# Optimization experiments

Hardware: AMD Instinct MI355X
Metric: run time of the kernel (lower is better)

The kernel has to match this reference:

```python
import jax, jax.numpy as jnp
import numpy as np

N = 50000
E = 800000
IN_CH = 128
HID = 16
HEADS = 16
OUT_CH = 64
NEG_SLOPE = 0.2
EPS = 1e-16


def _add_self_loops(edge_index, n):
    loops = jnp.arange(n, dtype=edge_index.dtype)
    src = jnp.concatenate([edge_index[0], loops])
    dst = jnp.concatenate([edge_index[1], loops])
    return src, dst


def gat_conv(x, src, dst, W, a_src, a_dst, b, heads, out_ch, concat, n):
    # x: [N, F_in], W: [F_in, heads*out_ch], a_src/a_dst: [heads, out_ch]
    h = (x @ W).reshape(n, heads, out_ch)                 # [N, H, C]
    alpha_src = jnp.sum(h * a_src, axis=-1)               # [N, H]
    alpha_dst = jnp.sum(h * a_dst, axis=-1)               # [N, H]
    e = alpha_src[src] + alpha_dst[dst]                   # [E, H]
    e = jnp.where(e > 0, e, NEG_SLOPE * e)                # LeakyReLU(0.2)
    m = jax.ops.segment_max(e, dst, num_segments=n)       # [N, H] (finite: self-loops)
    ex = jnp.exp(e - m[dst])                              # [E, H]
    denom = jax.ops.segment_sum(ex, dst, num_segments=n)  # [N, H]
    alpha = ex / (denom[dst] + EPS)                       # [E, H]
    msg = h[src] * alpha[:, :, None]                      # [E, H, C]
    out = jax.ops.segment_sum(msg, dst, num_segments=n)   # [N, H, C]
    if concat:
        out = out.reshape(n, heads * out_ch)
    else:
        out = out.mean(axis=1)
    return out + b


def setup_inputs() -> dict:
    key = jax.random.key(0)
    ks = jax.random.split(key, 10)
    x = jax.random.normal(ks[0], (N, IN_CH), dtype=jnp.float32)
    edge_index = jax.random.randint(ks[1], (2, E), 0, N, dtype=jnp.int64)
    s1 = 1.0 / np.sqrt(IN_CH)
    W1 = jax.random.normal(ks[2], (IN_CH, HEADS * HID), dtype=jnp.float32) * s1
    a_src1 = jax.random.normal(ks[3], (HEADS, HID), dtype=jnp.float32) * (1.0 / np.sqrt(HID))
    a_dst1 = jax.random.normal(ks[4], (HEADS, HID), dtype=jnp.float32) * (1.0 / np.sqrt(HID))
    b1 = jnp.zeros((HEADS * HID,), dtype=jnp.float32)
    s2 = 1.0 / np.sqrt(HEADS * HID)
    W2 = jax.random.normal(ks[5], (HEADS * HID, OUT_CH), dtype=jnp.float32) * s2
    a_src2 = jax.random.normal(ks[6], (1, OUT_CH), dtype=jnp.float32) * (1.0 / np.sqrt(OUT_CH))
    a_dst2 = jax.random.normal(ks[7], (1, OUT_CH), dtype=jnp.float32) * (1.0 / np.sqrt(OUT_CH))
    b2 = jnp.zeros((OUT_CH,), dtype=jnp.float32)
    return {"x": x, "edge_index": edge_index, "W1": W1, "a_src1": a_src1,
            "a_dst1": a_dst1, "b1": b1, "W2": W2, "a_src2": a_src2,
            "a_dst2": a_dst2, "b2": b2}


def reference(x, edge_index, W1, a_src1, a_dst1, b1, W2, a_src2, a_dst2, b2):
    src, dst = _add_self_loops(edge_index, N)
    h = gat_conv(x, src, dst, W1, a_src1, a_dst1, b1, HEADS, HID, True, N)
    h = gat_conv(h, src, dst, W2, a_src2, a_dst2, b2, 1, OUT_CH, False, N)
    return jax.nn.sigmoid(h)
```

## Files before the change

kernel.cpp:

```cpp
#include <hip/hip_runtime.h>
#include <hip/hip_bf16.h>

#define NN 50000
#define EE 800000
#define TE 850000
#define BK 64
#define NGB 782
#define NEB 1661

typedef __hip_bfloat16 bf16;
typedef __attribute__((ext_vector_type(8))) short short8v;
typedef __attribute__((ext_vector_type(4))) float float4v;

__device__ __forceinline__ float bu2f(unsigned short v) {
    return __uint_as_float((unsigned)v << 16);
}
__device__ __forceinline__ unsigned short f2bu(float v) {
    bf16 t = __float2bfloat16(v);
    return *(unsigned short*)&t;
}
__device__ __forceinline__ float lrelu(float e) { return (e > 0.f) ? e : 0.2f * e; }
__device__ __forceinline__ int clampn(int v) {
    return (v < 0) ? 0 : (v >= NN ? NN - 1 : v);
}

__global__ __launch_bounds__(256) void wprep_k(
    const float* __restrict__ W1, const float* __restrict__ W2,
    const float* __restrict__ asr1, const float* __restrict__ ads1,
    const float* __restrict__ asr2, const float* __restrict__ ads2,
    unsigned short* __restrict__ W1T, unsigned short* __restrict__ W2T,
    unsigned short* __restrict__ P1sT, unsigned short* __restrict__ P1dT,
    unsigned short* __restrict__ P2T, int* __restrict__ deg) {
    int b = blockIdx.x, t = threadIdx.x;
    for (int i = b * 256 + t; i < NN; i += 256 * 256) deg[i] = 0;
    if (b < 128) {
        int j = b * 256 + t;
        int n = j >> 7, k = j & 127;
        W1T[j] = f2bu(W1[k * 256 + n]);
    } else if (b < 192) {
        int j = (b - 128) * 256 + t;
        int n = j >> 8, k = j & 255;
        W2T[j] = f2bu(W2[k * 64 + n]);
    } else if (b == 192) {
        for (int j = t; j < 2048; j += 256) {
            int h = j >> 7, k = j & 127;
            float s = 0.f, d = 0.f;
            for (int c = 0; c < 16; ++c) {
                float wv = W1[k * 256 + h * 16 + c];
                s += wv * asr1[h * 16 + c];
                d += wv * ads1[h * 16 + c];
            }
            P1sT[j] = f2bu(s);
            P1dT[j] = f2bu(d);
        }
    } else if (b == 193) {
        int k = t;
        float s = 0.f, d = 0.f;
        for (int c = 0; c < 64; ++c) {
            float wv = W2[k * 64 + c];
            s += wv * asr2[c];
            d += wv * ads2[c];
        }
        P2T[k] = f2bu(s);
        P2T[256 + k] = f2bu(d);
        for (int j = 512 + t; j < 4096; j += 256) P2T[j] = 0;
    }
}

__global__ __launch_bounds__(256) void eg1_k(
    const void* __restrict__ ei, const float* __restrict__ x,
    const unsigned short* __restrict__ W1T,
    const unsigned short* __restrict__ P1sT, const unsigned short* __restrict__ P1dT,
    int* __restrict__ deg, int* __restrict__ csr,
    bf16* __restrict__ h1, float* __restrict__ a_src, float* __restrict__ a_dst) {
    if (blockIdx.x < NGB) {
        int wv = threadIdx.x >> 6, lane = threadIdx.x & 63;
        int m = lane & 15, quad = lane >> 4;
        int row0 = blockIdx.x * 64 + wv * 16;
        int arow = row0 + m;
        int arowc = (arow < NN) ? arow : NN - 1;
        const float4* x4 = (const float4*)x;
        short8v a[4];
#pragma unroll
        for (int ks = 0; ks < 4; ++ks) {
            float4 f0 = x4[(size_t)arowc * 32 + ks * 8 + quad * 2];
            float4 f1 = x4[(size_t)arowc * 32 + ks * 8 + quad * 2 + 1];
            union { short8v v; unsigned short u[8]; } ua;
            ua.u[0] = f2bu(f0.x); ua.u[1] = f2bu(f0.y);
            ua.u[2] = f2bu(f0.z); ua.u[3] = f2bu(f0.w);
            ua.u[4] = f2bu(f1.x); ua.u[5] = f2bu(f1.y);
            ua.u[6] = f2bu(f1.z); ua.u[7] = f2bu(f1.w);
            a[ks] = ua.v;
        }
        float4v accs = {0.f, 0.f, 0.f, 0.f}, accd = {0.f, 0.f, 0.f, 0.f};
#pragma unroll
        for (int ks = 0; ks < 4; ++ks) {
            short8v bs = *(const short8v*)&P1sT[(size_t)m * 128 + quad * 8 + ks * 32];
            short8v bd = *(const short8v*)&P1dT[(size_t)m * 128 + quad * 8 + ks * 32];
            accs = __builtin_amdgcn_mfma_f32_16x16x32_bf16(a[ks], bs, accs, 0, 0, 0);
            accd = __builtin_amdgcn_mfma_f32_16x16x32_bf16(a[ks], bd, accd, 0, 0, 0);
        }
        float4v acc[16];
#pragma unroll
        for (int t = 0; t < 16; ++t) {
            float4v c = {0.f, 0.f, 0.f, 0.f};
            const unsigned short* wb = &W1T[(size_t)(t * 16 + m) * 128 + quad * 8];
#pragma unroll
            for (int ks = 0; ks < 4; ++ks) {
                short8v b = *(const short8v*)&wb[ks * 32];
                c = __builtin_amdgcn_mfma_f32_16x16x32_bf16(a[ks], b, c, 0, 0, 0);
            }
            acc[t] = c;
        }
#pragma unroll
        for (int t = 0; t < 16; ++t) {
#pragma unroll
            for (int r = 0; r < 4; ++r) {
                int orow = row0 + quad * 4 + r;
                if (orow < NN)
                    h1[(size_t)orow * 256 + t * 16 + m] = __float2bfloat16(acc[t][r]);
            }
        }
#pragma unroll
        for (int r = 0; r < 4; ++r) {
            int orow = row0 + quad * 4 + r;
            if (orow < NN) {
                a_src[orow * 16 + m] = accs[r];
                a_dst[orow * 16 + m] = accd[r];
            }
        }
        return;
    }
    __shared__ int sflag;
    int t = threadIdx.x;
    if (t < 64) {
        unsigned z = (((const unsigned*)ei)[2 * t + 1] == 0u) ? 1u : 0u;
        unsigned long long mb = __ballot(z);
        if (t == 0) sflag = (__popcll(mb) >= 32) ? 1 : 0;
    }
    __syncthreads();
    int isi64 = sflag;
    int p = (blockIdx.x - NGB) * 256 + t;
    int i0 = p * 2;
    if (i0 >= TE) return;
    int s0, d0, s1 = -1, d1 = -1;
    if (i0 + 1 < EE) {
        if (isi64) {
            longlong2 sv = ((const longlong2*)ei)[p];
            longlong2 dv = ((const longlong2*)ei)[(EE >> 1) + p];
            s0 = clampn((int)sv.x); s1 = clampn((int)sv.y);
            d0 = clampn((int)dv.x); d1 = clampn((int)dv.y);
        } else {
            int2 sv = ((const int2*)ei)[p];
            int2 dv = ((const int2*)ei)[(EE >> 1) + p];
            s0 = clampn(sv.x); s1 = clampn(sv.y);
            d0 = clampn(dv.x); d1 = clampn(dv.y);
        }
    } else {
        auto lde = [&](long long idx) {
            return clampn(isi64 ? (int)((const long long*)ei)[idx] : ((const int*)ei)[idx]);
        };
        if (i0 < EE) { s0 = lde(i0); d0 = lde((long long)EE + i0); }
        else         { s0 = i0 - EE; d0 = i0 - EE; }
        if (i0 + 1 < TE) {
            if (i0 + 1 < EE) { s1 = lde(i0 + 1); d1 = lde((long long)EE + i0 + 1); }
            else             { s1 = i0 + 1 - EE; d1 = i0 + 1 - EE; }
        }
    }
    int pos0 = atomicAdd(&deg[d0], 1);
    if (pos0 < BK) csr[d0 * BK + pos0] = s0;
    if (d1 >= 0) {
        int pos1 = atomicAdd(&deg[d1], 1);
        if (pos1 < BK) csr[d1 * BK + pos1] = s1;
    }
}

__global__ __launch_bounds__(256) void agg1_k(
    const int* __restrict__ deg, int* __restrict__ csr,
    const float* __restrict__ a_src, const float* __restrict__ a_dst,
    const bf16* __restrict__ h1, const float* __restrict__ b1,
    bf16* __restrict__ out1) {
    __shared__ int sbuf[4][64];
    int wv = threadIdx.x >> 6, lane = threadIdx.x & 63;
    int dst = blockIdx.x * 4 + wv;
    int d = deg[dst]; if (d > BK) d = BK;
    int base = dst * BK;
    int v = (lane < d) ? csr[base + lane] : 0x7fffffff;
    int rank = 0;
    for (int j = 0; j < d; ++j) {
        int vj = __shfl(v, j, 64);
        rank += (vj < v || (vj == v && j < lane)) ? 1 : 0;
    }
    if (lane < d) sbuf[wv][rank] = v;
    if (lane < d) csr[base + lane] = sbuf[wv][lane];
    int we = lane >> 4, wh = lane & 15;
    int hc = lane >> 2;
    float adst_w = a_dst[dst * 16 + wh];
    float ax = 0.f, ay = 0.f, az = 0.f, aw = 0.f;
    float dsum = 0.f;
    int t0 = 0;
    for (; t0 + 4 <= d; t0 += 4) {
        int sr = sbuf[wv][t0 + we];
        float wr = __expf(lrelu(a_src[sr * 16 + wh] + adst_w));
        dsum += wr;
#pragma unroll
        for (int j = 0; j < 4; ++j) {
            float wj = __shfl(wr, j * 16 + hc, 64);
            int sj = sbuf[wv][t0 + j];
            ushort4 hv = *(const ushort4*)&h1[(size_t)sj * 256 + lane * 4];
            ax += wj * bu2f(hv.x);
            ay += wj * bu2f(hv.y);
            az += wj * bu2f(hv.z);
            aw += wj * bu2f(hv.w);
        }
    }
    if (t0 < d) {
        int n = d - t0;
        float wr = 0.f;
        if (we < n) {
            int sr = sbuf[wv][t0 + we];
            wr = __expf(lrelu(a_src[sr * 16 + wh] + adst_w));
        }
        dsum += wr;
        for (int j = 0; j < n; ++j) {
            float wj = __shfl(wr, j * 16 + hc, 64);
            int sj = sbuf[wv][t0 + j];
            ushort4 hv = *(const ushort4*)&h1[(size_t)sj * 256 + lane * 4];
            ax += wj * bu2f(hv.x);
            ay += wj * bu2f(hv.y);
            az += wj * bu2f(hv.z);
            aw += wj * bu2f(hv.w);
        }
    }
    dsum += __shfl_xor(dsum, 16, 64);
    dsum += __shfl_xor(dsum, 32, 64);
    float invd = 1.f / (__shfl(dsum, hc, 64) + 1e-16f);
    float4 bv = *(const float4*)&b1[lane * 4];
    ushort4 st;
    st.x = f2bu(ax * invd + bv.x);
    st.y = f2bu(ay * invd + bv.y);
    st.z = f2bu(az * invd + bv.z);
    st.w = f2bu(aw * invd + bv.w);
    *(ushort4*)&out1[(size_t)dst * 256 + lane * 4] = st;
}

__global__ __launch_bounds__(256) void gemm2_k(
    const bf16* __restrict__ out1, const unsigned short* __restrict__ W2T,
    const unsigned short* __restrict__ P2T,
    bf16* __restrict__ h2, float* __restrict__ a_src2, float* __restrict__ a_dst2) {
    int wv = threadIdx.x >> 6, lane = threadIdx.x & 63;
    int m = lane & 15, quad = lane >> 4;
    int row0 = blockIdx.x * 64 + wv * 16;
    int arow = row0 + m;
    int arowc = (arow < NN) ? arow : NN - 1;
    const unsigned short* ab = (const unsigned short*)out1;
    short8v a[8];
#pragma unroll
    for (int ks = 0; ks < 8; ++ks)
        a[ks] = *(const short8v*)&ab[(size_t)arowc * 256 + ks * 32 + quad * 8];
    float4v acca = {0.f, 0.f, 0.f, 0.f};
#pragma unroll
    for (int ks = 0; ks < 8; ++ks) {
        short8v b = *(const short8v*)&P2T[(size_t)m * 256 + quad * 8 + ks * 32];
        acca = __builtin_amdgcn_mfma_f32_16x16x32_bf16(a[ks], b, acca, 0, 0, 0);
    }
    float4v acc[4];
#pragma unroll
    for (int t = 0; t < 4; ++t) {
        float4v c = {0.f, 0.f, 0.f, 0.f};
        const unsigned short* wb = &W2T[(size_t)(t * 16 + m) * 256 + quad * 8];
#pragma unroll
        for (int ks = 0; ks < 8; ++ks) {
            short8v b = *(const short8v*)&wb[ks * 32];
            c = __builtin_amdgcn_mfma_f32_16x16x32_bf16(a[ks], b, c, 0, 0, 0);
        }
        acc[t] = c;
    }
#pragma unroll
    for (int t = 0; t < 4; ++t) {
#pragma unroll
        for (int r = 0; r < 4; ++r) {
            int orow = row0 + quad * 4 + r;
            if (orow < NN)
                h2[(size_t)orow * 64 + t * 16 + m] = __float2bfloat16(acc[t][r]);
        }
    }
#pragma unroll
    for (int r = 0; r < 4; ++r) {
        int orow = row0 + quad * 4 + r;
        if (orow < NN) {
            if (m == 0) a_src2[orow] = acca[r];
            if (m == 1) a_dst2[orow] = acca[r];
        }
    }
}

__global__ __launch_bounds__(256) void agg2_k(
    const int* __restrict__ deg, const int* __restrict__ csr,
    const float* __restrict__ a_src2, const float* __restrict__ a_dst2,
    const bf16* __restrict__ h2, const float* __restrict__ b2,
    float* __restrict__ out) {
    int wv = threadIdx.x >> 6;
    int lane = threadIdx.x & 63;
    int dst = blockIdx.x * 4 + wv;
    if (dst >= NN) return;
    int d = deg[dst]; if (d > BK) d = BK;
    int base = dst * BK;
    float adst = a_dst2[dst];
    int half = lane >> 5, hl = lane & 31;
    float acc0 = 0.f, acc1 = 0.f, dsum = 0.f;
    float wr = 0.f; int sr = 0;
    if (lane < d) {
        sr = csr[base + lane];
        wr = __expf(lrelu(a_src2[sr] + adst));
    }
    dsum += wr;
    for (int j0 = 0; j0 < d; j0 += 8) {
        ushort2 hv[4];
        float wj[4];
#pragma unroll
        for (int u = 0; u < 4; ++u) {
            int j = j0 + u * 2 + half;
            int jc = (j < d) ? j : 0;
            float w = __shfl(wr, jc, 64);
            int sj = __shfl(sr, jc, 64);
            wj[u] = (j < d) ? w : 0.f;
            hv[u] = *(const ushort2*)&h2[(size_t)sj * 64 + hl * 2];
        }
#pragma unroll
        for (int u = 0; u < 4; ++u) {
            acc0 += wj[u] * bu2f(hv[u].x);
            acc1 += wj[u] * bu2f(hv[u].y);
        }
    }
    acc0 += __shfl_xor(acc0, 32, 64);
    acc1 += __shfl_xor(acc1, 32, 64);
#pragma unroll
    for (int o = 32; o >= 1; o >>= 1) dsum += __shfl_xor(dsum, o, 64);
    if (half == 0) {
        float inv = 1.f / (dsum + 1e-16f);
        float o0 = acc0 * inv + b2[hl * 2];
        float o1 = acc1 * inv + b2[hl * 2 + 1];
        float2 st;
        st.x = 1.f / (1.f + __expf(-o0));
        st.y = 1.f / (1.f + __expf(-o1));
        *(float2*)&out[(size_t)dst * 64 + hl * 2] = st;
    }
}


extern "C" void kernel_launch(void* const* d_in, const int* in_sizes, int n_in,
                              void* d_out, int out_size, void* d_ws, size_t ws_size,
                              hipStream_t stream) {
    const float* x    = (const float*)d_in[0];
    const void*  ei   = d_in[1];
    const float* W1   = (const float*)d_in[2];
    const float* asr1 = (const float*)d_in[3];
    const float* ads1 = (const float*)d_in[4];
    const float* b1   = (const float*)d_in[5];
    const float* W2   = (const float*)d_in[6];
    const float* asr2 = (const float*)d_in[7];
    const float* ads2 = (const float*)d_in[8];
    const float* b2   = (const float*)d_in[9];
    float* out = (float*)d_out;

    char* w = (char*)d_ws;
    auto carve = [&](size_t bytes) {
        void* p = (void*)w;
        w += (bytes + 255) & ~(size_t)255;
        return p;
    };
    int*    csr      = (int*)carve((size_t)NN * BK * 4);
    int*    deg      = (int*)carve((size_t)NN * 4);
    float*  a_src1   = (float*)carve((size_t)NN * 16 * 4);
    float*  a_dst1   = (float*)carve((size_t)NN * 16 * 4);
    unsigned short* W1T  = (unsigned short*)carve(128 * 256 * 2);
    unsigned short* W2T  = (unsigned short*)carve(256 * 64 * 2);
    unsigned short* P1sT = (unsigned short*)carve(16 * 128 * 2);
    unsigned short* P1dT = (unsigned short*)carve(16 * 128 * 2);
    unsigned short* P2T  = (unsigned short*)carve(16 * 256 * 2);
    bf16*   h1       = (bf16*)carve((size_t)NN * 256 * 2);
    bf16*   out1     = (bf16*)carve((size_t)NN * 256 * 2);
    char*   l2base   = (char*)h1;
    bf16*   h2       = (bf16*)l2base;
    float*  a_src2   = (float*)(l2base + (size_t)NN * 64 * 2);
    float*  a_dst2   = a_src2 + NN;

    wprep_k<<<256, 256, 0, stream>>>(W1, W2, asr1, ads1, asr2, ads2,
                                     W1T, W2T, P1sT, P1dT, P2T, deg);
    eg1_k<<<NGB + NEB, 256, 0, stream>>>(ei, x, W1T, P1sT, P1dT,
                                         deg, csr, h1, a_src1, a_dst1);
    agg1_k<<<NN / 4, 256, 0, stream>>>(deg, csr, a_src1, a_dst1, h1, b1, out1);
    gemm2_k<<<(NN + 63) / 64, 256, 0, stream>>>(out1, W2T, P2T, h2, a_src2, a_dst2);
    agg2_k<<<(NN + 3) / 4, 256, 0, stream>>>(deg, csr, a_src2, a_dst2, h2, b2, out);
}
```

Baseline: 270.9 us.

## Fuse layer-1 aggregation and layer-2 GEMM with per-tile completion counters

```diff
diff --git a/kernel.cpp b/kernel.cpp
--- a/kernel.cpp
+++ b/kernel.cpp
@@ -7,6 +7,7 @@
 #define BK 64
 #define NGB 782
 #define NEB 1661
+#define NAB 12500
 
 typedef __hip_bfloat16 bf16;
 typedef __attribute__((ext_vector_type(8))) short short8v;
@@ -30,9 +31,12 @@
     const float* __restrict__ asr2, const float* __restrict__ ads2,
     unsigned short* __restrict__ W1T, unsigned short* __restrict__ W2T,
     unsigned short* __restrict__ P1sT, unsigned short* __restrict__ P1dT,
-    unsigned short* __restrict__ P2T, int* __restrict__ deg) {
+    unsigned short* __restrict__ P2T, int* __restrict__ deg,
+    int* __restrict__ cnt) {
     int b = blockIdx.x, t = threadIdx.x;
     for (int i = b * 256 + t; i < NN; i += 256 * 256) deg[i] = 0;
+    int ci = b * 256 + t;
+    if (ci < NGB) cnt[ci] = 0;
     if (b < 128) {
         int j = b * 256 + t;
         int n = j >> 7, k = j & 127;
@@ -175,82 +179,96 @@
     }
 }
 
-__global__ __launch_bounds__(256) void agg1_k(
+__global__ __launch_bounds__(256) void eg2_k(
     const int* __restrict__ deg, int* __restrict__ csr,
     const float* __restrict__ a_src, const float* __restrict__ a_dst,
     const bf16* __restrict__ h1, const float* __restrict__ b1,
-    bf16* __restrict__ out1) {
-    __shared__ int sbuf[4][64];
+    bf16* __restrict__ out1,
+    const unsigned short* __restrict__ W2T, const unsigned short* __restrict__ P2T,
+    bf16* __restrict__ h2, float* __restrict__ a_src2, float* __restrict__ a_dst2,
+    int* __restrict__ cnt) {
     int wv = threadIdx.x >> 6, lane = threadIdx.x & 63;
-    int dst = blockIdx.x * 4 + wv;
-    int d = deg[dst]; if (d > BK) d = BK;
-    int base = dst * BK;
-    int v = (lane < d) ? csr[base + lane] : 0x7fffffff;
-    int rank = 0;
-    for (int j = 0; j < d; ++j) {
-        int vj = __shfl(v, j, 64);
-        rank += (vj < v || (vj == v && j < lane)) ? 1 : 0;
-    }
-    if (lane < d) sbuf[wv][rank] = v;
-    if (lane < d) csr[base + lane] = sbuf[wv][lane];
-    int we = lane >> 4, wh = lane & 15;
-    int hc = lane >> 2;
-    float adst_w = a_dst[dst * 16 + wh];
-    float ax = 0.f, ay = 0.f, az = 0.f, aw = 0.f;
-    float dsum = 0.f;
-    int t0 = 0;
-    for (; t0 + 4 <= d; t0 += 4) {
-        int sr = sbuf[wv][t0 + we];
-        float wr = __expf(lrelu(a_src[sr * 16 + wh] + adst_w));
-        dsum += wr;
-#pragma unroll
-        for (int j = 0; j < 4; ++j) {
-            float wj = __shfl(wr, j * 16 + hc, 64);
-            int sj = sbuf[wv][t0 + j];
-            ushort4 hv = *(const ushort4*)&h1[(size_t)sj * 256 + lane * 4];
-            ax += wj * bu2f(hv.x);
-            ay += wj * bu2f(hv.y);
-            az += wj * bu2f(hv.z);
-            aw += wj * bu2f(hv.w);
-        }
-    }
-    if (t0 < d) {
-        int n = d - t0;
-        float wr = 0.f;
-        if (we < n) {
+    if (blockIdx.x < NAB) {
+        __shared__ int sbuf[4][64];
+        int dst = blockIdx.x * 4 + wv;
+        int d = deg[dst]; if (d > BK) d = BK;
+        int base = dst * BK;
+        int v = (lane < d) ? csr[base + lane] : 0x7fffffff;
+        int rank = 0;
+        for (int j = 0; j < d; ++j) {
+            int vj = __shfl(v, j, 64);
+            rank += (vj < v || (vj == v && j < lane)) ? 1 : 0;
+        }
+        if (lane < d) sbuf[wv][rank] = v;
+        if (lane < d) csr[base + lane] = sbuf[wv][lane];
+        int we = lane >> 4, wh = lane & 15;
+        int hc = lane >> 2;
+        float adst_w = a_dst[dst * 16 + wh];
+        float ax = 0.f, ay = 0.f, az = 0.f, aw = 0.f;
+        float dsum = 0.f;
+        int t0 = 0;
+        for (; t0 + 4 <= d; t0 += 4) {
             int sr = sbuf[wv][t0 + we];
-            wr = __expf(lrelu(a_src[sr * 16 + wh] + adst_w));
-        }
-        dsum += wr;
-        for (int j = 0; j < n; ++j) {
-            float wj = __shfl(wr, j * 16 + hc, 64);
-            int sj = sbuf[wv][t0 + j];
-            ushort4 hv = *(const ushort4*)&h1[(size_t)sj * 256 + lane * 4];
-            ax += wj * bu2f(hv.x);
-            ay += wj * bu2f(hv.y);
-            az += wj * bu2f(hv.z);
-            aw += wj * bu2f(hv.w);
-        }
-    }
-    dsum += __shfl_xor(dsum, 16, 64);
-    dsum += __shfl_xor(dsum, 32, 64);
-    float invd = 1.f / (__shfl(dsum, hc, 64) + 1e-16f);
-    float4 bv = *(const float4*)&b1[lane * 4];
-    ushort4 st;
-    st.x = f2bu(ax * invd + bv.x);
-    st.y = f2bu(ay * invd + bv.y);
-    st.z = f2bu(az * invd + bv.z);
-    st.w = f2bu(aw * invd + bv.w);
-    *(ushort4*)&out1[(size_t)dst * 256 + lane * 4] = st;
-}
-
-__global__ __launch_bounds__(256) void gemm2_k(
-    const bf16* __restrict__ out1, const unsigned short* __restrict__ W2T,
-    const unsigned short* __restrict__ P2T,
-    bf16* __restrict__ h2, float* __restrict__ a_src2, float* __restrict__ a_dst2) {
-    int wv = threadIdx.x >> 6, lane = threadIdx.x & 63;
+            float wr = __expf(lrelu(a_src[sr * 16 + wh] + adst_w));
+            dsum += wr;
+#pragma unroll
+            for (int j = 0; j < 4; ++j) {
+                float wj = __shfl(wr, j * 16 + hc, 64);
+                int sj = sbuf[wv][t0 + j];
+                ushort4 hv = *(const ushort4*)&h1[(size_t)sj * 256 + lane * 4];
+                ax += wj * bu2f(hv.x);
+                ay += wj * bu2f(hv.y);
+                az += wj * bu2f(hv.z);
+                aw += wj * bu2f(hv.w);
+            }
+        }
+        if (t0 < d) {
+            int n = d - t0;
+            float wr = 0.f;
+            if (we < n) {
+                int sr = sbuf[wv][t0 + we];
+                wr = __expf(lrelu(a_src[sr * 16 + wh] + adst_w));
+            }
+            dsum += wr;
+            for (int j = 0; j < n; ++j) {
+                float wj = __shfl(wr, j * 16 + hc, 64);
+                int sj = sbuf[wv][t0 + j];
+                ushort4 hv = *(const ushort4*)&h1[(size_t)sj * 256 + lane * 4];
+                ax += wj * bu2f(hv.x);
+                ay += wj * bu2f(hv.y);
+                az += wj * bu2f(hv.z);
+                aw += wj * bu2f(hv.w);
+            }
+        }
+        dsum += __shfl_xor(dsum, 16, 64);
+        dsum += __shfl_xor(dsum, 32, 64);
+        float invd = 1.f / (__shfl(dsum, hc, 64) + 1e-16f);
+        float4 bv = *(const float4*)&b1[lane * 4];
+        ushort4 st;
+        st.x = f2bu(ax * invd + bv.x);
+        st.y = f2bu(ay * invd + bv.y);
+        st.z = f2bu(az * invd + bv.z);
+        st.w = f2bu(aw * invd + bv.w);
+        *(ushort4*)&out1[(size_t)dst * 256 + lane * 4] = st;
+        __syncthreads();
+        if (threadIdx.x == 0) {
+            __threadfence();
+            __hip_atomic_fetch_add(&cnt[blockIdx.x >> 4], 1,
+                                   __ATOMIC_RELEASE, __HIP_MEMORY_SCOPE_AGENT);
+        }
+        return;
+    }
+    int jb = blockIdx.x - NAB;
+    if (threadIdx.x == 0) {
+        int target = NAB - jb * 16; if (target > 16) target = 16;
+        while (__hip_atomic_load(&cnt[jb], __ATOMIC_ACQUIRE,
+                                 __HIP_MEMORY_SCOPE_AGENT) < target)
+            __builtin_amdgcn_s_sleep(8);
+        __threadfence();
+    }
+    __syncthreads();
     int m = lane & 15, quad = lane >> 4;
-    int row0 = blockIdx.x * 64 + wv * 16;
+    int row0 = jb * 64 + wv * 16;
     int arow = row0 + m;
     int arowc = (arow < NN) ? arow : NN - 1;
     const unsigned short* ab = (const unsigned short*)out1;
@@ -372,6 +390,7 @@
     };
     int*    csr      = (int*)carve((size_t)NN * BK * 4);
     int*    deg      = (int*)carve((size_t)NN * 4);
+    int*    cnt      = (int*)carve((size_t)NGB * 4);
     float*  a_src1   = (float*)carve((size_t)NN * 16 * 4);
     float*  a_dst1   = (float*)carve((size_t)NN * 16 * 4);
     unsigned short* W1T  = (unsigned short*)carve(128 * 256 * 2);
@@ -381,16 +400,15 @@
     unsigned short* P2T  = (unsigned short*)carve(16 * 256 * 2);
     bf16*   h1       = (bf16*)carve((size_t)NN * 256 * 2);
     bf16*   out1     = (bf16*)carve((size_t)NN * 256 * 2);
-    char*   l2base   = (char*)h1;
-    bf16*   h2       = (bf16*)l2base;
-    float*  a_src2   = (float*)(l2base + (size_t)NN * 64 * 2);
-    float*  a_dst2   = a_src2 + NN;
+    bf16*   h2       = (bf16*)carve((size_t)NN * 64 * 2);
+    float*  a_src2   = (float*)carve((size_t)NN * 4);
+    float*  a_dst2   = (float*)carve((size_t)NN * 4);
 
     wprep_k<<<256, 256, 0, stream>>>(W1, W2, asr1, ads1, asr2, ads2,
-                                     W1T, W2T, P1sT, P1dT, P2T, deg);
+                                     W1T, W2T, P1sT, P1dT, P2T, deg, cnt);
     eg1_k<<<NGB + NEB, 256, 0, stream>>>(ei, x, W1T, P1sT, P1dT,
                                          deg, csr, h1, a_src1, a_dst1);
-    agg1_k<<<NN / 4, 256, 0, stream>>>(deg, csr, a_src1, a_dst1, h1, b1, out1);
-    gemm2_k<<<(NN + 63) / 64, 256, 0, stream>>>(out1, W2T, P2T, h2, a_src2, a_dst2);
+    eg2_k<<<NAB + NGB, 256, 0, stream>>>(deg, csr, a_src1, a_dst1, h1, b1, out1,
+                                         W2T, P2T, h2, a_src2, a_dst2, cnt);
     agg2_k<<<(NN + 3) / 4, 256, 0, stream>>>(deg, csr, a_src2, a_dst2, h2, b2, out);
 }
```

After: 958.1 us. +253.7%, slower.
